# Kernel optimization log

Measured on AMD Instinct MI355X. Metric: run time of the kernel, lower is better.

Reference implementation:

```python
import jax, jax.numpy as jnp
import numpy as np

D_MODEL = 1024
NUM_HEADS = 16
HEAD_DIM = D_MODEL // NUM_HEADS
BATCH = 2048


def setup_inputs() -> dict:
    key = jax.random.key(0)
    ks = jax.random.split(key, 11)
    s = 1.0 / np.sqrt(D_MODEL)
    inp = {
        "q": jax.random.normal(ks[0], (BATCH, D_MODEL), jnp.float32),
        "k": jax.random.normal(ks[1], (BATCH, D_MODEL), jnp.float32),
        "v": jax.random.normal(ks[2], (BATCH, D_MODEL), jnp.float32),
        "Wq": jax.random.normal(ks[3], (D_MODEL, D_MODEL), jnp.float32) * s,
        "bq": jnp.zeros((D_MODEL,), jnp.float32),
        "Wk": jax.random.normal(ks[4], (D_MODEL, D_MODEL), jnp.float32) * s,
        "bk": jnp.zeros((D_MODEL,), jnp.float32),
        "Wv": jax.random.normal(ks[5], (D_MODEL, D_MODEL), jnp.float32) * s,
        "bv": jnp.zeros((D_MODEL,), jnp.float32),
        "Wo": jax.random.normal(ks[6], (D_MODEL, D_MODEL), jnp.float32) * s,
        "bo": jnp.zeros((D_MODEL,), jnp.float32),
    }
    return inp


def reference(q, k, v, Wq, bq, Wk, bk, Wv, bv, Wo, bo):
    b = q.shape[0]
    # linear projections (torch Linear: x @ W.T + b)
    qh = (q @ Wq.T + bq).reshape(b, NUM_HEADS, HEAD_DIM).transpose(1, 0, 2)  # (h, b, dh)
    kh = (k @ Wk.T + bk).reshape(b, NUM_HEADS, HEAD_DIM).transpose(1, 0, 2)  # (h, b, dh)
    # attention across the batch dimension: (h, b, b)
    scores = jnp.einsum('hid,hjd->hij', qh, kh) / jnp.sqrt(jnp.float32(HEAD_DIM))
    attn = jax.nn.softmax(scores, axis=-1)
    # pool_method == 'mean': v stays full-width, mean over heads
    vp = v @ Wv.T + bv                               # (b, d_model)
    out = jnp.einsum('hij,jd->hid', attn, vp)        # (h, b, d_model)
    out = out.mean(axis=0)                           # (b, d_model)
    out = out @ Wo.T + bo
    return out
```

## Files before the change

kernel.cpp:

```cpp
#include <hip/hip_runtime.h>
#include <hip/hip_bf16.h>
#include <stdint.h>

#define D_MODEL 1024
#define NUM_HEADS 16
#define HEAD_DIM 64
#define BATCH 2048

typedef unsigned short u16;
typedef __bf16 bf16x8 __attribute__((ext_vector_type(8)));
typedef float f32x4 __attribute__((ext_vector_type(4)));
typedef u16 u16x8 __attribute__((ext_vector_type(8)));

typedef __attribute__((address_space(1))) void gv_t;
typedef __attribute__((address_space(3))) void lv_t;

__device__ __forceinline__ u16 f2bf(float f) {
    uint32_t u = __builtin_bit_cast(uint32_t, f);
    return (u16)((u + 0x7fffu + ((u >> 16) & 1u)) >> 16);
}
__device__ __forceinline__ f32x4 fzero4() { f32x4 v = {0.f, 0.f, 0.f, 0.f}; return v; }

template<int N> __device__ __forceinline__ void waitv() {
    if constexpr (N == 0) asm volatile("s_waitcnt vmcnt(0)" ::: "memory");
    else if constexpr (N == 2) asm volatile("s_waitcnt vmcnt(2)" ::: "memory");
    else if constexpr (N == 3) asm volatile("s_waitcnt vmcnt(3)" ::: "memory");
    else if constexpr (N == 4) asm volatile("s_waitcnt vmcnt(4)" ::: "memory");
    else if constexpr (N == 6) asm volatile("s_waitcnt vmcnt(6)" ::: "memory");
}
#define BAR() do { __builtin_amdgcn_s_barrier(); __builtin_amdgcn_sched_barrier(0); } while (0)

struct Conv7 {
    const float* src[7];
    u16* dst[7];
    int n[7];
};

__global__ __launch_bounds__(256) void convert_kernel(Conv7 a) {
    const int y = blockIdx.y;
    const int n = a.n[y];
    const long base = (long)(blockIdx.x * 256 + threadIdx.x) * 8;
    if (base >= n) return;
    const float* s = a.src[y] + base;
    const float4 f0 = *(const float4*)s;
    const float4 f1 = *(const float4*)(s + 4);
    u16x8 o;
    o[0] = f2bf(f0.x); o[1] = f2bf(f0.y); o[2] = f2bf(f0.z); o[3] = f2bf(f0.w);
    o[4] = f2bf(f1.x); o[5] = f2bf(f1.y); o[6] = f2bf(f1.z); o[7] = f2bf(f1.w);
    *(u16x8*)(a.dst[y] + base) = o;
}

struct G3 {
    const u16* A[3];
    const u16* Bt[3];
    const float* bias[3];
    void* C[3];
    int trans[3];
    int ldc[3];
};

__global__ __launch_bounds__(256, 3) void proj128_kernel(G3 g, int K) {
    __shared__ __align__(16) u16 As[3][128 * 32];
    __shared__ __align__(16) u16 Bs[3][128 * 32];
    const int z = blockIdx.z;
    const u16* __restrict__ A = g.A[z];
    const u16* __restrict__ Bt = g.Bt[z];
    const int tid = threadIdx.x, lane = tid & 63, wid = tid >> 6;
    const int l15 = lane & 15, l4 = lane >> 4;
    const int wr = wid >> 1, wc = wid & 1;
    const size_t brow = blockIdx.x, bcol = blockIdx.y;
    const int trow = tid >> 2;
    const int cswz = ((tid & 3) ^ (trow & 3)) * 8;
    const int sa = l15 & 3;

    const u16* Ag = A + (brow * 128 + trow) * (size_t)K + cswz;
    const u16* Bg = Bt + (bcol * 128 + trow) * (size_t)K + cswz;

    f32x4 acc[4][4];
#pragma unroll
    for (int m = 0; m < 4; m++)
#pragma unroll
        for (int n = 0; n < 4; n++) acc[m][n] = fzero4();

#define STGP(bi, k0) do { \
        __builtin_amdgcn_global_load_lds((gv_t*)(Ag + (k0)), (lv_t*)(&As[bi][tid * 8]), 16, 0, 0); \
        __builtin_amdgcn_global_load_lds((gv_t*)(Ag + (size_t)64 * K + (k0)), (lv_t*)(&As[bi][tid * 8 + 2048]), 16, 0, 0); \
        __builtin_amdgcn_global_load_lds((gv_t*)(Bg + (k0)), (lv_t*)(&Bs[bi][tid * 8]), 16, 0, 0); \
        __builtin_amdgcn_global_load_lds((gv_t*)(Bg + (size_t)64 * K + (k0)), (lv_t*)(&Bs[bi][tid * 8 + 2048]), 16, 0, 0); \
    } while (0)

    const int NT = K / 32;
    STGP(0, 0);
    STGP(1, 32);
    int cur = 0, pf = 2;
    for (int t = 0; t < NT; ++t) {
        if (t + 1 < NT) waitv<4>(); else waitv<0>();
        BAR();
        bf16x8 a[4], b[4];
#pragma unroll
        for (int m = 0; m < 4; m++) {
            const int row = wr * 64 + m * 16 + l15;
            a[m] = *(const bf16x8*)&As[cur][row * 32 + ((l4 ^ sa) * 8)];
        }
#pragma unroll
        for (int n = 0; n < 4; n++) {
            const int row = wc * 64 + n * 16 + l15;
            b[n] = *(const bf16x8*)&Bs[cur][row * 32 + ((l4 ^ sa) * 8)];
        }
        if (t + 2 < NT) STGP(pf, (t + 2) * 32);
        __builtin_amdgcn_s_setprio(1);
#pragma unroll
        for (int m = 0; m < 4; m++)
#pragma unroll
            for (int n = 0; n < 4; n++)
                acc[m][n] = __builtin_amdgcn_mfma_f32_16x16x32_bf16(a[m], b[n], acc[m][n], 0, 0, 0);
        __builtin_amdgcn_s_setprio(0);
        cur = (cur == 2) ? 0 : cur + 1;
        pf = (pf == 2) ? 0 : pf + 1;
    }
#undef STGP

    const int trans = g.trans[z];
    const size_t ldc = g.ldc[z];
    const float* bias = g.bias[z];
#pragma unroll
    for (int m = 0; m < 4; m++)
#pragma unroll
        for (int n = 0; n < 4; n++) {
            const size_t col = bcol * 128 + wc * 64 + n * 16 + l15;
            const float bv = bias[col];
#pragma unroll
            for (int j = 0; j < 4; j++) {
                const size_t row = brow * 128 + wr * 64 + m * 16 + l4 * 4 + j;
                const float val = acc[m][n][j] + bv;
                const size_t idx = trans ? (col * ldc + row) : (row * ldc + col);
                ((u16*)g.C[z])[idx] = f2bf(val);
            }
        }
}

template<int OUT_BF16, int HAS_BIAS>
__global__ __launch_bounds__(256, 2) void gemm64(G3 g, int K) {
    __shared__ __align__(16) u16 As[3][128 * 64];
    __shared__ __align__(16) u16 Bs[3][64 * 64];
    const int z = blockIdx.z;
    const u16* __restrict__ A = g.A[z];
    const u16* __restrict__ Bt = g.Bt[z];
    const int tid = threadIdx.x, lane = tid & 63, wid = tid >> 6;
    const int l15 = lane & 15, l4 = lane >> 4;
    const int wr = wid >> 1, wc = wid & 1;
    const size_t brow = blockIdx.x, bcol = blockIdx.y;
    const int trow = tid >> 3;
    const int cswz = ((tid & 7) ^ (trow & 7)) * 8;
    const int sa = l15 & 7;

    const u16* Ag = A + (brow * 128 + trow) * (size_t)K + cswz;
    const u16* Bg = Bt + (bcol * 64 + trow) * (size_t)K + cswz;

    f32x4 acc[4][2];
#pragma unroll
    for (int m = 0; m < 4; m++)
#pragma unroll
        for (int n = 0; n < 2; n++) acc[m][n] = fzero4();

#define STG64(bi, k0) do { \
        __builtin_amdgcn_global_load_lds((gv_t*)(Ag + (k0)), (lv_t*)(&As[bi][tid * 8]), 16, 0, 0); \
        __builtin_amdgcn_global_load_lds((gv_t*)(Ag + (size_t)32 * K + (k0)), (lv_t*)(&As[bi][tid * 8 + 2048]), 16, 0, 0); \
        __builtin_amdgcn_global_load_lds((gv_t*)(Ag + (size_t)64 * K + (k0)), (lv_t*)(&As[bi][tid * 8 + 4096]), 16, 0, 0); \
        __builtin_amdgcn_global_load_lds((gv_t*)(Ag + (size_t)96 * K + (k0)), (lv_t*)(&As[bi][tid * 8 + 6144]), 16, 0, 0); \
        __builtin_amdgcn_global_load_lds((gv_t*)(Bg + (k0)), (lv_t*)(&Bs[bi][tid * 8]), 16, 0, 0); \
        __builtin_amdgcn_global_load_lds((gv_t*)(Bg + (size_t)32 * K + (k0)), (lv_t*)(&Bs[bi][tid * 8 + 2048]), 16, 0, 0); \
    } while (0)

    const int NT = K / 64;
    STG64(0, 0);
    STG64(1, 64);
    int cur = 0, pf = 2;
    for (int t = 0; t < NT; ++t) {
        if (t + 1 < NT) waitv<6>(); else waitv<0>();
        BAR();
        bf16x8 a[4][2], b[2][2];
#pragma unroll
        for (int m = 0; m < 4; m++)
#pragma unroll
            for (int kk = 0; kk < 2; kk++)
                a[m][kk] = *(const bf16x8*)&As[cur][(wr * 64 + m * 16 + l15) * 64 + (((kk * 4 + l4) ^ sa) * 8)];
#pragma unroll
        for (int n = 0; n < 2; n++)
#pragma unroll
            for (int kk = 0; kk < 2; kk++)
                b[n][kk] = *(const bf16x8*)&Bs[cur][(wc * 32 + n * 16 + l15) * 64 + (((kk * 4 + l4) ^ sa) * 8)];
        if (t + 2 < NT) STG64(pf, (t + 2) * 64);
        __builtin_amdgcn_s_setprio(1);
#pragma unroll
        for (int m = 0; m < 4; m++)
#pragma unroll
            for (int n = 0; n < 2; n++) {
                acc[m][n] = __builtin_amdgcn_mfma_f32_16x16x32_bf16(a[m][0], b[n][0], acc[m][n], 0, 0, 0);
                acc[m][n] = __builtin_amdgcn_mfma_f32_16x16x32_bf16(a[m][1], b[n][1], acc[m][n], 0, 0, 0);
            }
        __builtin_amdgcn_s_setprio(0);
        cur = (cur == 2) ? 0 : cur + 1;
        pf = (pf == 2) ? 0 : pf + 1;
    }
#undef STG64

    const int trans = g.trans[z];
    const size_t ldc = g.ldc[z];
    const float* bias = g.bias[z];
#pragma unroll
    for (int m = 0; m < 4; m++)
#pragma unroll
        for (int n = 0; n < 2; n++) {
            const size_t col = bcol * 64 + wc * 32 + n * 16 + l15;
            const float bv = HAS_BIAS ? bias[col] : 0.f;
#pragma unroll
            for (int j = 0; j < 4; j++) {
                const size_t row = brow * 128 + wr * 64 + m * 16 + l4 * 4 + j;
                const float val = acc[m][n][j] + bv;
                if (OUT_BF16) {
                    const size_t idx = trans ? (col * ldc + row) : (row * ldc + col);
                    ((u16*)g.C[z])[idx] = f2bf(val);
                } else {
                    ((float*)g.C[z])[row * ldc + col] = val;
                }
            }
        }
}

__global__ __launch_bounds__(256, 2) void rowsum_kernel(
    const u16* __restrict__ Q, const u16* __restrict__ Kb, float* __restrict__ inv)
{
    __shared__ __align__(16) u16 Qs[2][64 * 32];
    __shared__ __align__(16) u16 Ks[3][2][64 * 32];
    const int tid = threadIdx.x, lane = tid & 63, wid = tid >> 6;
    const int l15 = lane & 15, l4 = lane >> 4;
    const int h = blockIdx.y;
    const size_t r0 = (size_t)blockIdx.x * 64;
    const int srow = tid >> 2;
    const int scol = (tid & 3) * 8;

#define STGR(bi, it) do { \
        __builtin_amdgcn_global_load_lds( \
            (gv_t*)(Kb + ((size_t)(it) * 64 + srow) * D_MODEL + h * HEAD_DIM + scol), \
            (lv_t*)(Ks[bi][0] + tid * 8), 16, 0, 0); \
        __builtin_amdgcn_global_load_lds( \
            (gv_t*)(Kb + ((size_t)(it) * 64 + srow) * D_MODEL + h * HEAD_DIM + 32 + scol), \
            (lv_t*)(Ks[bi][1] + tid * 8), 16, 0, 0); \
    } while (0)

#pragma unroll
    for (int kk = 0; kk < 2; kk++)
        __builtin_amdgcn_global_load_lds(
            (gv_t*)(Q + (r0 + srow) * D_MODEL + h * HEAD_DIM + kk * 32 + scol),
            (lv_t*)(Qs[kk] + tid * 8), 16, 0, 0);
    STGR(0, 0);
    STGR(1, 1);
    waitv<4>();
    BAR();
    bf16x8 aq[2];
#pragma unroll
    for (int kk = 0; kk < 2; kk++)
        aq[kk] = *(const bf16x8*)&Qs[kk][(wid * 16 + l15) * 32 + l4 * 8];

    float psum[4] = {0.f, 0.f, 0.f, 0.f};
    const int NT = BATCH / 64;
    int cur = 0, pf = 2;
    for (int it = 0; it < NT; ++it) {
        if (it + 1 < NT) waitv<2>(); else waitv<0>();
        BAR();
        bf16x8 b0[4], b1[4];
#pragma unroll
        for (int n = 0; n < 4; n++) {
            b0[n] = *(const bf16x8*)&Ks[cur][0][(n * 16 + l15) * 32 + l4 * 8];
            b1[n] = *(const bf16x8*)&Ks[cur][1][(n * 16 + l15) * 32 + l4 * 8];
        }
        if (it + 2 < NT) STGR(pf, it + 2);
        __builtin_amdgcn_s_setprio(1);
        f32x4 s[4];
#pragma unroll
        for (int n = 0; n < 4; n++) {
            s[n] = fzero4();
            s[n] = __builtin_amdgcn_mfma_f32_16x16x32_bf16(aq[0], b0[n], s[n], 0, 0, 0);
            s[n] = __builtin_amdgcn_mfma_f32_16x16x32_bf16(aq[1], b1[n], s[n], 0, 0, 0);
        }
        __builtin_amdgcn_s_setprio(0);
#pragma unroll
        for (int n = 0; n < 4; n++)
#pragma unroll
            for (int j = 0; j < 4; j++) psum[j] += __expf(s[n][j] * 0.125f);
        cur = (cur == 2) ? 0 : cur + 1;
        pf = (pf == 2) ? 0 : pf + 1;
    }
#undef STGR
#pragma unroll
    for (int off = 8; off >= 1; off >>= 1)
#pragma unroll
        for (int j = 0; j < 4; j++) psum[j] += __shfl_xor(psum[j], off, 64);
    if (l15 == 0) {
#pragma unroll
        for (int j = 0; j < 4; j++)
            inv[(size_t)h * BATCH + r0 + wid * 16 + l4 * 4 + j] = 1.0f / (16.0f * psum[j]);
    }
}

__global__ __launch_bounds__(256, 2) void amean_kernel(
    const u16* __restrict__ Q, const u16* __restrict__ Kb,
    const float* __restrict__ inv, u16* __restrict__ Am)
{
    __shared__ __align__(16) u16 As[3][128 * 64];
    __shared__ __align__(16) u16 Bs[3][64 * 64];
    const int tid = threadIdx.x, lane = tid & 63, wid = tid >> 6;
    const int l15 = lane & 15, l4 = lane >> 4;
    const int wr = wid >> 1, wc = wid & 1;
    const size_t brow = blockIdx.x, bcol = blockIdx.y;
    const int trow = tid >> 3;
    const int cswz = ((tid & 7) ^ (trow & 7)) * 8;
    const int sa = l15 & 7;

    const u16* Ag = Q + (brow * 128 + trow) * (size_t)D_MODEL + cswz;
    const u16* Bg = Kb + (bcol * 64 + trow) * (size_t)D_MODEL + cswz;

#define STGM(bi, k0) do { \
        __builtin_amdgcn_global_load_lds((gv_t*)(Ag + (k0)), (lv_t*)(&As[bi][tid * 8]), 16, 0, 0); \
        __builtin_amdgcn_global_load_lds((gv_t*)(Ag + (size_t)32 * D_MODEL + (k0)), (lv_t*)(&As[bi][tid * 8 + 2048]), 16, 0, 0); \
        __builtin_amdgcn_global_load_lds((gv_t*)(Ag + (size_t)64 * D_MODEL + (k0)), (lv_t*)(&As[bi][tid * 8 + 4096]), 16, 0, 0); \
        __builtin_amdgcn_global_load_lds((gv_t*)(Ag + (size_t)96 * D_MODEL + (k0)), (lv_t*)(&As[bi][tid * 8 + 6144]), 16, 0, 0); \
        __builtin_amdgcn_global_load_lds((gv_t*)(Bg + (k0)), (lv_t*)(&Bs[bi][tid * 8]), 16, 0, 0); \
        __builtin_amdgcn_global_load_lds((gv_t*)(Bg + (size_t)32 * D_MODEL + (k0)), (lv_t*)(&Bs[bi][tid * 8 + 2048]), 16, 0, 0); \
    } while (0)

    float accA[4][2][4] = {};
    STGM(0, 0);
    STGM(1, 64);
    int cur = 0, pf = 2;
    const float SC = 0.125f * 1.44269504088896341f;

    for (int h = 0; h < NUM_HEADS; h++) {
        if (h + 1 < NUM_HEADS) waitv<6>(); else waitv<0>();
        BAR();
        bf16x8 a[4][2], b[2][2];
#pragma unroll
        for (int m = 0; m < 4; m++)
#pragma unroll
            for (int kk = 0; kk < 2; kk++)
                a[m][kk] = *(const bf16x8*)&As[cur][(wr * 64 + m * 16 + l15) * 64 + (((kk * 4 + l4) ^ sa) * 8)];
#pragma unroll
        for (int n = 0; n < 2; n++)
#pragma unroll
            for (int kk = 0; kk < 2; kk++)
                b[n][kk] = *(const bf16x8*)&Bs[cur][(wc * 32 + n * 16 + l15) * 64 + (((kk * 4 + l4) ^ sa) * 8)];
        if (h + 2 < NUM_HEADS) STGM(pf, (h + 2) * 64);
        __builtin_amdgcn_s_setprio(1);
        f32x4 acc[4][2];
#pragma unroll
        for (int m = 0; m < 4; m++)
#pragma unroll
            for (int n = 0; n < 2; n++) {
                acc[m][n] = fzero4();
                acc[m][n] = __builtin_amdgcn_mfma_f32_16x16x32_bf16(a[m][0], b[n][0], acc[m][n], 0, 0, 0);
                acc[m][n] = __builtin_amdgcn_mfma_f32_16x16x32_bf16(a[m][1], b[n][1], acc[m][n], 0, 0, 0);
            }
        __builtin_amdgcn_s_setprio(0);
#pragma unroll
        for (int m = 0; m < 4; m++) {
            const f32x4 iv = *(const f32x4*)&inv[(size_t)h * BATCH + brow * 128 + wr * 64 + m * 16 + l4 * 4];
#pragma unroll
            for (int n = 0; n < 2; n++)
#pragma unroll
                for (int j = 0; j < 4; j++)
                    accA[m][n][j] += exp2f(acc[m][n][j] * SC) * iv[j];
        }
        cur = (cur == 2) ? 0 : cur + 1;
        pf = (pf == 2) ? 0 : pf + 1;
    }
#undef STGM

#pragma unroll
    for (int m = 0; m < 4; m++)
#pragma unroll
        for (int n = 0; n < 2; n++)
#pragma unroll
            for (int j = 0; j < 4; j++) {
                const size_t row = brow * 128 + wr * 64 + m * 16 + l4 * 4 + j;
                const size_t col = bcol * 64 + wc * 32 + n * 16 + l15;
                Am[row * (size_t)BATCH + col] = f2bf(accA[m][n][j]);
            }
}

extern "C" void kernel_launch(void* const* d_in, const int* in_sizes, int n_in,
                              void* d_out, int out_size, void* d_ws, size_t ws_size,
                              hipStream_t stream)
{
    const float* q  = (const float*)d_in[0];
    const float* k  = (const float*)d_in[1];
    const float* v  = (const float*)d_in[2];
    const float* Wq = (const float*)d_in[3];
    const float* bq = (const float*)d_in[4];
    const float* Wk = (const float*)d_in[5];
    const float* bk = (const float*)d_in[6];
    const float* Wv = (const float*)d_in[7];
    const float* bv = (const float*)d_in[8];
    const float* Wo = (const float*)d_in[9];
    const float* bo = (const float*)d_in[10];
    float* out = (float*)d_out;

    char* p = (char*)d_ws;
    u16* qb  = (u16*)p; p += (size_t)BATCH * D_MODEL * 2;
    u16* kb  = (u16*)p; p += (size_t)BATCH * D_MODEL * 2;
    u16* vb  = (u16*)p; p += (size_t)BATCH * D_MODEL * 2;
    u16* wqb = (u16*)p; p += (size_t)D_MODEL * D_MODEL * 2;
    u16* wkb = (u16*)p; p += (size_t)D_MODEL * D_MODEL * 2;
    u16* wvb = (u16*)p; p += (size_t)D_MODEL * D_MODEL * 2;
    u16* wob = (u16*)p; p += (size_t)D_MODEL * D_MODEL * 2;
    u16* Qb  = (u16*)p; p += (size_t)BATCH * D_MODEL * 2;
    u16* Kp  = (u16*)p; p += (size_t)BATCH * D_MODEL * 2;
    u16* VPt = (u16*)p; p += (size_t)D_MODEL * BATCH * 2;
    u16* Am  = (u16*)p; p += (size_t)BATCH * BATCH * 2;
    u16* T   = (u16*)p; p += (size_t)BATCH * D_MODEL * 2;
    float* inv = (float*)p;

    Conv7 ca;
    ca.src[0] = q;  ca.dst[0] = qb;  ca.n[0] = BATCH * D_MODEL;
    ca.src[1] = k;  ca.dst[1] = kb;  ca.n[1] = BATCH * D_MODEL;
    ca.src[2] = v;  ca.dst[2] = vb;  ca.n[2] = BATCH * D_MODEL;
    ca.src[3] = Wq; ca.dst[3] = wqb; ca.n[3] = D_MODEL * D_MODEL;
    ca.src[4] = Wk; ca.dst[4] = wkb; ca.n[4] = D_MODEL * D_MODEL;
    ca.src[5] = Wv; ca.dst[5] = wvb; ca.n[5] = D_MODEL * D_MODEL;
    ca.src[6] = Wo; ca.dst[6] = wob; ca.n[6] = D_MODEL * D_MODEL;
    convert_kernel<<<dim3(1024, 7), 256, 0, stream>>>(ca);

    G3 pr;
    pr.A[0] = qb; pr.Bt[0] = wqb; pr.bias[0] = bq; pr.C[0] = Qb;  pr.trans[0] = 0; pr.ldc[0] = D_MODEL;
    pr.A[1] = kb; pr.Bt[1] = wkb; pr.bias[1] = bk; pr.C[1] = Kp;  pr.trans[1] = 0; pr.ldc[1] = D_MODEL;
    pr.A[2] = vb; pr.Bt[2] = wvb; pr.bias[2] = bv; pr.C[2] = VPt; pr.trans[2] = 1; pr.ldc[2] = BATCH;
    proj128_kernel<<<dim3(16, 8, 3), 256, 0, stream>>>(pr, D_MODEL);

    rowsum_kernel<<<dim3(BATCH / 64, NUM_HEADS), 256, 0, stream>>>(Qb, Kp, inv);
    amean_kernel<<<dim3(BATCH / 128, BATCH / 64), 256, 0, stream>>>(Qb, Kp, inv, Am);

    G3 gt;
    gt.A[0] = Am; gt.Bt[0] = VPt; gt.bias[0] = nullptr; gt.C[0] = T; gt.trans[0] = 0; gt.ldc[0] = D_MODEL;
    gt.A[1] = gt.A[0]; gt.Bt[1] = gt.Bt[0]; gt.bias[1] = nullptr; gt.C[1] = gt.C[0]; gt.trans[1] = 0; gt.ldc[1] = D_MODEL;
    gt.A[2] = gt.A[0]; gt.Bt[2] = gt.Bt[0]; gt.bias[2] = nullptr; gt.C[2] = gt.C[0]; gt.trans[2] = 0; gt.ldc[2] = D_MODEL;
    gemm64<1, 0><<<dim3(16, 16, 1), 256, 0, stream>>>(gt, BATCH);

    G3 go;
    go.A[0] = T; go.Bt[0] = wob; go.bias[0] = bo; go.C[0] = out; go.trans[0] = 0; go.ldc[0] = D_MODEL;
    go.A[1] = go.A[0]; go.Bt[1] = go.Bt[0]; go.bias[1] = go.bias[0]; go.C[1] = go.C[0]; go.trans[1] = 0; go.ldc[1] = D_MODEL;
    go.A[2] = go.A[0]; go.Bt[2] = go.Bt[0]; go.bias[2] = go.bias[0]; go.C[2] = go.C[0]; go.trans[2] = 0; go.ldc[2] = D_MODEL;
    gemm64<0, 1><<<dim3(16, 16, 1), 256, 0, stream>>>(go, D_MODEL);
}
```

Before: 118.6 us.

## Reassociate output projection: precompute Wo·VPᵀ in attention kernel, drop one GEMM

Uses associativity to compute U = Wo·VPᵀ (1024x2048) inside the attention-mean kernel as extra blocks, then runs a single Am·Uᵀ GEMM with K=2048 plus bias. This replaces the sequential Am·VP then T·Woᵀ GEMMs. One kernel launch and the intermediate T round trip go away, and the U GEMM overlaps with the attention-matrix blocks. The trade-offs are that the final GEMM now has K=2048 instead of 1024, and bf16 rounding of U changes the numerics slightly.

New measurement: 106.4 us. -10.3%, faster.

```diff
diff --git a/kernel.cpp b/kernel.cpp
--- a/kernel.cpp
+++ b/kernel.cpp
@@ -24,7 +24,6 @@
 template<int N> __device__ __forceinline__ void waitv() {
     if constexpr (N == 0) asm volatile("s_waitcnt vmcnt(0)" ::: "memory");
     else if constexpr (N == 2) asm volatile("s_waitcnt vmcnt(2)" ::: "memory");
-    else if constexpr (N == 3) asm volatile("s_waitcnt vmcnt(3)" ::: "memory");
     else if constexpr (N == 4) asm volatile("s_waitcnt vmcnt(4)" ::: "memory");
     else if constexpr (N == 6) asm volatile("s_waitcnt vmcnt(6)" ::: "memory");
 }
@@ -304,20 +303,91 @@
     }
 }
 
-__global__ __launch_bounds__(256, 2) void amean_kernel(
+__global__ __launch_bounds__(256, 2) void ameanu_kernel(
     const u16* __restrict__ Q, const u16* __restrict__ Kb,
-    const float* __restrict__ inv, u16* __restrict__ Am)
+    const float* __restrict__ inv, u16* __restrict__ Am,
+    const u16* __restrict__ wob, const u16* __restrict__ VP, u16* __restrict__ Ut)
 {
     __shared__ __align__(16) u16 As[3][128 * 64];
     __shared__ __align__(16) u16 Bs[3][64 * 64];
     const int tid = threadIdx.x, lane = tid & 63, wid = tid >> 6;
     const int l15 = lane & 15, l4 = lane >> 4;
     const int wr = wid >> 1, wc = wid & 1;
-    const size_t brow = blockIdx.x, bcol = blockIdx.y;
+    const int bx = blockIdx.x, by = blockIdx.y;
     const int trow = tid >> 3;
     const int cswz = ((tid & 7) ^ (trow & 7)) * 8;
     const int sa = l15 & 7;
 
+    if (by >= 32) {
+        const size_t brow = bx >> 1;
+        const size_t bcol = (size_t)(by - 32) * 2 + (bx & 1);
+        const int K = D_MODEL;
+        const u16* Ag = wob + (brow * 128 + trow) * (size_t)K + cswz;
+        const u16* Bg = VP + (bcol * 64 + trow) * (size_t)K + cswz;
+
+        f32x4 acc[4][2];
+#pragma unroll
+        for (int m = 0; m < 4; m++)
+#pragma unroll
+            for (int n = 0; n < 2; n++) acc[m][n] = fzero4();
+
+#define STGU(bi, k0) do { \
+        __builtin_amdgcn_global_load_lds((gv_t*)(Ag + (k0)), (lv_t*)(&As[bi][tid * 8]), 16, 0, 0); \
+        __builtin_amdgcn_global_load_lds((gv_t*)(Ag + (size_t)32 * K + (k0)), (lv_t*)(&As[bi][tid * 8 + 2048]), 16, 0, 0); \
+        __builtin_amdgcn_global_load_lds((gv_t*)(Ag + (size_t)64 * K + (k0)), (lv_t*)(&As[bi][tid * 8 + 4096]), 16, 0, 0); \
+        __builtin_amdgcn_global_load_lds((gv_t*)(Ag + (size_t)96 * K + (k0)), (lv_t*)(&As[bi][tid * 8 + 6144]), 16, 0, 0); \
+        __builtin_amdgcn_global_load_lds((gv_t*)(Bg + (k0)), (lv_t*)(&Bs[bi][tid * 8]), 16, 0, 0); \
+        __builtin_amdgcn_global_load_lds((gv_t*)(Bg + (size_t)32 * K + (k0)), (lv_t*)(&Bs[bi][tid * 8 + 2048]), 16, 0, 0); \
+    } while (0)
+
+        const int NT = K / 64;
+        STGU(0, 0);
+        STGU(1, 64);
+        int cur = 0, pf = 2;
+        for (int t = 0; t < NT; ++t) {
+            if (t + 1 < NT) waitv<6>(); else waitv<0>();
+            BAR();
+            bf16x8 a[4][2], b[2][2];
+#pragma unroll
+            for (int m = 0; m < 4; m++)
+#pragma unroll
+                for (int kk = 0; kk < 2; kk++)
+                    a[m][kk] = *(const bf16x8*)&As[cur][(wr * 64 + m * 16 + l15) * 64 + (((kk * 4 + l4) ^ sa) * 8)];
+#pragma unroll
+            for (int n = 0; n < 2; n++)
+#pragma unroll
+                for (int kk = 0; kk < 2; kk++)
+                    b[n][kk] = *(const bf16x8*)&Bs[cur][(wc * 32 + n * 16 + l15) * 64 + (((kk * 4 + l4) ^ sa) * 8)];
+            if (t + 2 < NT) STGU(pf, (t + 2) * 64);
+            __builtin_amdgcn_s_setprio(1);
+#pragma unroll
+            for (int m = 0; m < 4; m++)
+#pragma unroll
+                for (int n = 0; n < 2; n++) {
+                    acc[m][n] = __builtin_amdgcn_mfma_f32_16x16x32_bf16(a[m][0], b[n][0], acc[m][n], 0, 0, 0);
+                    acc[m][n] = __builtin_amdgcn_mfma_f32_16x16x32_bf16(a[m][1], b[n][1], acc[m][n], 0, 0, 0);
+                }
+            __builtin_amdgcn_s_setprio(0);
+            cur = (cur == 2) ? 0 : cur + 1;
+            pf = (pf == 2) ? 0 : pf + 1;
+        }
+#undef STGU
+
+#pragma unroll
+        for (int m = 0; m < 4; m++)
+#pragma unroll
+            for (int n = 0; n < 2; n++) {
+                const size_t col = bcol * 64 + wc * 32 + n * 16 + l15;
+#pragma unroll
+                for (int j = 0; j < 4; j++) {
+                    const size_t row = brow * 128 + wr * 64 + m * 16 + l4 * 4 + j;
+                    Ut[row * (size_t)BATCH + col] = f2bf(acc[m][n][j]);
+                }
+            }
+        return;
+    }
+
+    const size_t brow = bx, bcol = by;
     const u16* Ag = Q + (brow * 128 + trow) * (size_t)D_MODEL + cswz;
     const u16* Bg = Kb + (bcol * 64 + trow) * (size_t)D_MODEL + cswz;
 
@@ -415,9 +485,9 @@
     u16* wob = (u16*)p; p += (size_t)D_MODEL * D_MODEL * 2;
     u16* Qb  = (u16*)p; p += (size_t)BATCH * D_MODEL * 2;
     u16* Kp  = (u16*)p; p += (size_t)BATCH * D_MODEL * 2;
-    u16* VPt = (u16*)p; p += (size_t)D_MODEL * BATCH * 2;
+    u16* VP  = (u16*)p; p += (size_t)BATCH * D_MODEL * 2;
     u16* Am  = (u16*)p; p += (size_t)BATCH * BATCH * 2;
-    u16* T   = (u16*)p; p += (size_t)BATCH * D_MODEL * 2;
+    u16* Ut  = (u16*)p; p += (size_t)D_MODEL * BATCH * 2;
     float* inv = (float*)p;
 
     Conv7 ca;
@@ -431,23 +501,18 @@
     convert_kernel<<<dim3(1024, 7), 256, 0, stream>>>(ca);
 
     G3 pr;
-    pr.A[0] = qb; pr.Bt[0] = wqb; pr.bias[0] = bq; pr.C[0] = Qb;  pr.trans[0] = 0; pr.ldc[0] = D_MODEL;
-    pr.A[1] = kb; pr.Bt[1] = wkb; pr.bias[1] = bk; pr.C[1] = Kp;  pr.trans[1] = 0; pr.ldc[1] = D_MODEL;
-    pr.A[2] = vb; pr.Bt[2] = wvb; pr.bias[2] = bv; pr.C[2] = VPt; pr.trans[2] = 1; pr.ldc[2] = BATCH;
+    pr.A[0] = qb; pr.Bt[0] = wqb; pr.bias[0] = bq; pr.C[0] = Qb; pr.trans[0] = 0; pr.ldc[0] = D_MODEL;
+    pr.A[1] = kb; pr.Bt[1] = wkb; pr.bias[1] = bk; pr.C[1] = Kp; pr.trans[1] = 0; pr.ldc[1] = D_MODEL;
+    pr.A[2] = vb; pr.Bt[2] = wvb; pr.bias[2] = bv; pr.C[2] = VP; pr.trans[2] = 0; pr.ldc[2] = D_MODEL;
     proj128_kernel<<<dim3(16, 8, 3), 256, 0, stream>>>(pr, D_MODEL);
 
     rowsum_kernel<<<dim3(BATCH / 64, NUM_HEADS), 256, 0, stream>>>(Qb, Kp, inv);
-    amean_kernel<<<dim3(BATCH / 128, BATCH / 64), 256, 0, stream>>>(Qb, Kp, inv, Am);
-
-    G3 gt;
-    gt.A[0] = Am; gt.Bt[0] = VPt; gt.bias[0] = nullptr; gt.C[0] = T; gt.trans[0] = 0; gt.ldc[0] = D_MODEL;
-    gt.A[1] = gt.A[0]; gt.Bt[1] = gt.Bt[0]; gt.bias[1] = nullptr; gt.C[1] = gt.C[0]; gt.trans[1] = 0; gt.ldc[1] = D_MODEL;
-    gt.A[2] = gt.A[0]; gt.Bt[2] = gt.Bt[0]; gt.bias[2] = nullptr; gt.C[2] = gt.C[0]; gt.trans[2] = 0; gt.ldc[2] = D_MODEL;
-    gemm64<1, 0><<<dim3(16, 16, 1), 256, 0, stream>>>(gt, BATCH);
+
+    ameanu_kernel<<<dim3(16, 48), 256, 0, stream>>>(Qb, Kp, inv, Am, wob, VP, Ut);
 
     G3 go;
-    go.A[0] = T; go.Bt[0] = wob; go.bias[0] = bo; go.C[0] = out; go.trans[0] = 0; go.ldc[0] = D_MODEL;
+    go.A[0] = Am; go.Bt[0] = Ut; go.bias[0] = bo; go.C[0] = out; go.trans[0] = 0; go.ldc[0] = D_MODEL;
     go.A[1] = go.A[0]; go.Bt[1] = go.Bt[0]; go.bias[1] = go.bias[0]; go.C[1] = go.C[0]; go.trans[1] = 0; go.ldc[1] = D_MODEL;
     go.A[2] = go.A[0]; go.Bt[2] = go.Bt[0]; go.bias[2] = go.bias[0]; go.C[2] = go.C[0]; go.trans[2] = 0; go.ldc[2] = D_MODEL;
-    gemm64<0, 1><<<dim3(16, 16, 1), 256, 0, stream>>>(go, D_MODEL);
-}
+    gemm64<0, 1><<<dim3(16, 16, 1), 256, 0, stream>>>(go, BATCH);
+}
```
